# Performance work log

Hardware: AMD Instinct MI355X
Metric: run time of the kernel (lower is better)

Reference implementation:

```python
import jax, jax.numpy as jnp
import numpy as np

N_DRUG = 50000
N_DIS = 50000
N_EDGES = 500000
IN_UNITS = 4096   # rows of basis-decomposed weight (index vocab)
MSG_SMALL = 128   # msg_units(384) // 3 (ini=True)
OUT_UNITS = 256
BASIS_UNITS = 4
N_RATINGS = 2


def setup_inputs() -> dict:
    key = jax.random.key(0)
    ks = jax.random.split(key, 12)
    inp = {
        "drug_feat": jax.random.randint(ks[0], (N_DRUG, 3), 0, IN_UNITS, dtype=jnp.int32),
        "dis_feat": jax.random.randint(ks[1], (N_DIS, 3), 0, IN_UNITS, dtype=jnp.int32),
        # edge_src[r] = drug endpoint, edge_dst[r] = disease endpoint of rating-r edges
        "edge_src": jax.random.randint(ks[2], (N_RATINGS, N_EDGES), 0, N_DRUG, dtype=jnp.int32),
        "edge_dst": jax.random.randint(ks[3], (N_RATINGS, N_EDGES), 0, N_DIS, dtype=jnp.int32),
        # degree normalizers (graph.srcdata['cj'] / dstdata['ci'])
        "cj_drug": jax.random.uniform(ks[4], (N_DRUG, 1), dtype=jnp.float32),
        "ci_drug": jax.random.uniform(ks[5], (N_DRUG, 1), dtype=jnp.float32),
        "cj_dis": jax.random.uniform(ks[6], (N_DIS, 1), dtype=jnp.float32),
        "ci_dis": jax.random.uniform(ks[7], (N_DIS, 1), dtype=jnp.float32),
        # learned params (share_user_item_param=True -> ifc is ufc)
        "att": jax.random.normal(ks[8], (N_RATINGS, BASIS_UNITS), dtype=jnp.float32),
        "basis": jax.random.normal(ks[9], (BASIS_UNITS, IN_UNITS, MSG_SMALL), dtype=jnp.float32) * 0.02,
        "fc_w": jax.random.normal(ks[10], (OUT_UNITS, 3 * MSG_SMALL), dtype=jnp.float32) * 0.05,
        "fc_b": jnp.zeros((OUT_UNITS,), dtype=jnp.float32),
    }
    return inp


def _gather_feat(idx, Wr):
    # dot_or_identity: concat(W[idx0], W[idx1], W[idx2]) -> [N, 3*msg_small]
    g = Wr[idx]                      # [N, 3, msg_small]
    return g.reshape(idx.shape[0], -1)


def reference(drug_feat, dis_feat, edge_src, edge_dst, cj_drug, ci_drug,
              cj_dis, ci_dis, att, basis, fc_w, fc_b):
    # basis decomposition: W = att @ basis.view(B,-1) -> [R, in_units, msg_small]
    W = jnp.einsum('rb,bim->rim', att, basis)
    drug_out = jnp.zeros((cj_drug.shape[0], 3 * W.shape[2]), dtype=W.dtype)
    dis_out = jnp.zeros((cj_dis.shape[0], 3 * W.shape[2]), dtype=W.dtype)
    for r in range(att.shape[0]):
        Wr = W[r]
        src, dst = edge_src[r], edge_dst[r]
        # rating edges: drug -> disease (copy_src + sum, then * ci)
        h_drug = _gather_feat(drug_feat, Wr) * cj_drug
        dis_out = dis_out + jax.ops.segment_sum(h_drug[src], dst,
                                                num_segments=cj_dis.shape[0])
        # rev-rating edges: disease -> drug
        h_dis = _gather_feat(dis_feat, Wr) * cj_dis
        drug_out = drug_out + jax.ops.segment_sum(h_dis[dst], src,
                                                  num_segments=cj_drug.shape[0])
    dis_out = dis_out * ci_dis
    drug_out = drug_out * ci_drug
    # agg_act=None (identity), dropout_rate=0; shared output projection
    drug_out = drug_out @ fc_w.T + fc_b   # ifc
    dis_out = dis_out @ fc_w.T + fc_b     # ufc (shared params)
    return drug_out, dis_out
```

## Files before the change

### kernel.cpp

```cpp
#include <hip/hip_runtime.h>
#include <hip/hip_bf16.h>

#define N_NODE   50000
#define N_EDGES  500000
#define IN_UNITS 4096
#define MSG      128
#define OUT      256
#define N_RAT    2
#define CAP      64
#define NBKT     782
#define BCAP     2048
#define STAGE    8

typedef float f32x4 __attribute__((ext_vector_type(4)));

__device__ inline float bf2f(unsigned short u) {
    return __uint_as_float(((unsigned int)u) << 16);
}
__device__ inline unsigned short f2bf(float f) {
    unsigned int x = __float_as_uint(f);
    return (unsigned short)((x + 0x7fff + ((x >> 16) & 1)) >> 16);
}

__global__ void zero_kernel(int* p, int n) {
    int i = blockIdx.x * 256 + threadIdx.x;
    if (i < n) p[i] = 0;
}

__global__ void zw_kernel(const float* __restrict__ att,
                          const float* __restrict__ basis,
                          float* __restrict__ W,
                          int* __restrict__ bcnt) {
    int idx = blockIdx.x * 256 + threadIdx.x;
    if (blockIdx.x == 0) {
        for (int i = threadIdx.x; i < 2 * NBKT; i += 256) bcnt[i] = 0;
    }
    int r   = idx >> 19;
    int off = idx & 524287;
    float s = 0.f;
#pragma unroll
    for (int b = 0; b < 4; ++b)
        s += att[r * 4 + b] * basis[(size_t)b * 524288 + off];
    W[idx] = s;
}

template <typename OT>
__global__ __launch_bounds__(256) void p_kernel(const float* __restrict__ W,
                                                const float* __restrict__ fc_w,
                                                OT* __restrict__ P) {
    int t = blockIdx.z;
    int r = t / 3, k = t - r * 3;
    int i0 = blockIdx.y * 64;
    int o0 = blockIdx.x * 64;
    const float* A = W + (size_t)r * 4096 * 128;

    __shared__ float As[64][68];
    __shared__ float Bs[64][68];

    int tid = threadIdx.x;
    int tx = tid & 15, ty = tid >> 4;
    float acc[4][4] = {};

    for (int kk = 0; kk < 128; kk += 64) {
#pragma unroll
        for (int j = 0; j < 16; ++j) {
            int flat = tid + j * 256;
            int m = flat & 63, row = flat >> 6;
            As[m][row] = A[(size_t)(i0 + row) * 128 + kk + m];
            Bs[m][row] = fc_w[(size_t)(o0 + row) * 384 + k * 128 + kk + m];
        }
        __syncthreads();
#pragma unroll 8
        for (int m = 0; m < 64; ++m) {
            float4 a = *(const float4*)&As[m][ty * 4];
            float4 b = *(const float4*)&Bs[m][tx * 4];
            float av[4] = {a.x, a.y, a.z, a.w};
            float bv[4] = {b.x, b.y, b.z, b.w};
#pragma unroll
            for (int q = 0; q < 4; ++q)
#pragma unroll
                for (int p = 0; p < 4; ++p)
                    acc[q][p] += av[q] * bv[p];
        }
        __syncthreads();
    }
#pragma unroll
    for (int q = 0; q < 4; ++q) {
        size_t base = ((size_t)t * 4096 + i0 + ty * 4 + q) * 256 + o0 + tx * 4;
        if constexpr (sizeof(OT) == 4) {
            float4 v = make_float4(acc[q][0], acc[q][1], acc[q][2], acc[q][3]);
            *(float4*)&P[base] = v;
        } else {
            ushort4 v;
            v.x = f2bf(acc[q][0]); v.y = f2bf(acc[q][1]);
            v.z = f2bf(acc[q][2]); v.w = f2bf(acc[q][3]);
            *(ushort4*)&P[base] = v;
        }
    }
}

__global__ __launch_bounds__(256) void bin_kernel(
    const int* __restrict__ esrc, const int* __restrict__ edst,
    int* __restrict__ bcnt, int* __restrict__ bedges) {
    __shared__ int stage[2 * NBKT * STAGE];
    __shared__ int lcnt[2 * NBKT];
    int tid = threadIdx.x;
    for (int i = tid; i < 2 * NBKT; i += 256) lcnt[i] = 0;
    __syncthreads();

    const int EPB = (N_RAT * N_EDGES + gridDim.x - 1) / gridDim.x;
    int e0 = blockIdx.x * EPB;
    int e1 = e0 + EPB; if (e1 > N_RAT * N_EDGES) e1 = N_RAT * N_EDGES;

    for (int e = e0 + tid; e < e1; e += 256) {
        int r = (e >= N_EDGES) ? 1 : 0;
        int s = __builtin_nontemporal_load(esrc + e);
        int d = __builtin_nontemporal_load(edst + e);
        {
            int b = (s >> 6);
            int pay = d | (r << 16) | ((s & 63) << 17);
            int pos = atomicAdd(&lcnt[b], 1);
            if (pos < STAGE) stage[b * STAGE + pos] = pay;
            else { int gp = atomicAdd(&bcnt[b], 1);
                   if (gp < BCAP) bedges[(size_t)b * BCAP + gp] = pay; }
        }
        {
            int b = NBKT + (d >> 6);
            int pay = s | (r << 16) | ((d & 63) << 17);
            int pos = atomicAdd(&lcnt[b], 1);
            if (pos < STAGE) stage[b * STAGE + pos] = pay;
            else { int gp = atomicAdd(&bcnt[b], 1);
                   if (gp < BCAP) bedges[(size_t)b * BCAP + gp] = pay; }
        }
    }
    __syncthreads();
    for (int b = tid; b < 2 * NBKT; b += 256) {
        int n = lcnt[b]; if (n == 0) continue;
        if (n > STAGE) n = STAGE;
        int base = atomicAdd(&bcnt[b], n);
        for (int j = 0; j < n; ++j) {
            int pos = base + j;
            if (pos < BCAP) bedges[(size_t)b * BCAP + pos] = stage[b * STAGE + j];
        }
    }
}

__global__ __launch_bounds__(256) void hpre_kernel(
    const int* __restrict__ drug_feat, const int* __restrict__ dis_feat,
    const float* __restrict__ cj_drug, const float* __restrict__ cj_dis,
    const unsigned short* __restrict__ Pb, unsigned short* __restrict__ h) {
    int wave = blockIdx.x * 4 + (threadIdx.x >> 6);
    int lane = threadIdx.x & 63;
    if (wave >= 4 * N_NODE) return;
    int type = wave / (2 * N_NODE);
    int rem  = wave - type * 2 * N_NODE;
    int r    = rem / N_NODE;
    int node = rem - r * N_NODE;
    const int* feat = type ? dis_feat : drug_feat;
    float c = (type ? cj_dis : cj_drug)[node];
    int f0 = feat[node * 3 + 0];
    int f1 = feat[node * 3 + 1];
    int f2 = feat[node * 3 + 2];
    const ushort4* r0 = (const ushort4*)(Pb + (((size_t)(r * 3 + 0) * 4096 + f0) << 8));
    const ushort4* r1 = (const ushort4*)(Pb + (((size_t)(r * 3 + 1) * 4096 + f1) << 8));
    const ushort4* r2 = (const ushort4*)(Pb + (((size_t)(r * 3 + 2) * 4096 + f2) << 8));
    ushort4 a = r0[lane], b = r1[lane], d = r2[lane];
    ushort4 o;
    o.x = f2bf(c * (bf2f(a.x) + bf2f(b.x) + bf2f(d.x)));
    o.y = f2bf(c * (bf2f(a.y) + bf2f(b.y) + bf2f(d.y)));
    o.z = f2bf(c * (bf2f(a.z) + bf2f(b.z) + bf2f(d.z)));
    o.w = f2bf(c * (bf2f(a.w) + bf2f(b.w) + bf2f(d.w)));
    ((ushort4*)(h + ((size_t)wave << 8)))[lane] = o;
}

__global__ __launch_bounds__(256) void accum5_kernel(
    const int* __restrict__ bcnt, const int* __restrict__ bedges,
    const float* __restrict__ ci_drug, const float* __restrict__ ci_dis,
    const unsigned short* __restrict__ h, const float* __restrict__ fc_b,
    float* __restrict__ out) {
    __shared__ int slots[64][CAP];
    __shared__ int scnt[64];
    int tid = threadIdx.x;
    int b = blockIdx.x;
    int side = (b >= NBKT) ? 1 : 0;
    int bk = side ? b - NBKT : b;
    int node0 = bk * 64;

    if (tid < 64) scnt[tid] = 0;
    __syncthreads();

    int n = bcnt[b]; if (n > BCAP) n = BCAP;
    for (int i = tid; i < n; i += 256) {
        int pay = __builtin_nontemporal_load(bedges + (size_t)b * BCAP + i);
        int ln = (pay >> 17) & 63;
        int p = atomicAdd(&scnt[ln], 1);
        if (p < CAP) slots[ln][p] = pay;
    }
    __syncthreads();

    int wid = tid >> 6, lane = tid & 63;
    const float* ci = side ? ci_dis : ci_drug;
    int hoff = side ? 0 : 2 * N_NODE;
    float4 bv = ((const float4*)fc_b)[lane];

    for (int ln = wid; ln < 64; ln += 4) {
        int node = node0 + ln;
        if (node >= N_NODE) continue;
        int m = scnt[ln]; if (m > CAP) m = CAP;
        float4 acc = make_float4(0.f, 0.f, 0.f, 0.f);
        int j = 0;
        for (; j + 4 <= m; j += 4) {
            int p0 = slots[ln][j+0], p1 = slots[ln][j+1];
            int p2 = slots[ln][j+2], p3 = slots[ln][j+3];
            const ushort4* r0 = (const ushort4*)(h +
                ((size_t)(hoff + ((p0 >> 16) & 1) * N_NODE + (p0 & 0xFFFF)) << 8));
            const ushort4* r1 = (const ushort4*)(h +
                ((size_t)(hoff + ((p1 >> 16) & 1) * N_NODE + (p1 & 0xFFFF)) << 8));
            const ushort4* r2 = (const ushort4*)(h +
                ((size_t)(hoff + ((p2 >> 16) & 1) * N_NODE + (p2 & 0xFFFF)) << 8));
            const ushort4* r3 = (const ushort4*)(h +
                ((size_t)(hoff + ((p3 >> 16) & 1) * N_NODE + (p3 & 0xFFFF)) << 8));
            ushort4 v0 = r0[lane], v1 = r1[lane], v2 = r2[lane], v3 = r3[lane];
            acc.x += (bf2f(v0.x) + bf2f(v1.x)) + (bf2f(v2.x) + bf2f(v3.x));
            acc.y += (bf2f(v0.y) + bf2f(v1.y)) + (bf2f(v2.y) + bf2f(v3.y));
            acc.z += (bf2f(v0.z) + bf2f(v1.z)) + (bf2f(v2.z) + bf2f(v3.z));
            acc.w += (bf2f(v0.w) + bf2f(v1.w)) + (bf2f(v2.w) + bf2f(v3.w));
        }
        for (; j < m; ++j) {
            int pay = slots[ln][j];
            const ushort4* hr = (const ushort4*)(h +
                ((size_t)(hoff + ((pay >> 16) & 1) * N_NODE + (pay & 0xFFFF)) << 8));
            ushort4 v = hr[lane];
            acc.x += bf2f(v.x);
            acc.y += bf2f(v.y);
            acc.z += bf2f(v.z);
            acc.w += bf2f(v.w);
        }
        float civ = ci[node];
        float* orow = out + ((size_t)(side * N_NODE + node)) * 256;
        f32x4 res = {acc.x * civ + bv.x, acc.y * civ + bv.y,
                     acc.z * civ + bv.z, acc.w * civ + bv.w};
        __builtin_nontemporal_store(res, (f32x4*)orow + lane);
    }
}

__global__ void count_kernel(const int* __restrict__ esrc, const int* __restrict__ edst,
                             int* cnt_drug, int* cnt_dis) {
    int g = blockIdx.x * 256 + threadIdx.x;
    if (g >= N_RAT * N_EDGES) return;
    atomicAdd(&cnt_drug[esrc[g]], 1);
    atomicAdd(&cnt_dis[edst[g]], 1);
}

__global__ __launch_bounds__(1024) void scan_kernel(const int* cnt_drug, const int* cnt_dis,
                                                    int* offs_drug, int* offs_dis,
                                                    int* cur_drug, int* cur_dis) {
    const int n = N_NODE, chunk = 49;
    const int* cnt = blockIdx.x ? cnt_dis : cnt_drug;
    int* offs = blockIdx.x ? offs_dis : offs_drug;
    int* cur  = blockIdx.x ? cur_dis  : cur_drug;
    __shared__ int lds[1024];
    int t = threadIdx.x;
    int s = 0;
    int base = t * chunk;
    for (int j = 0; j < chunk; ++j) { int i = base + j; if (i < n) s += cnt[i]; }
    lds[t] = s;
    __syncthreads();
    for (int off = 1; off < 1024; off <<= 1) {
        int v = (t >= off) ? lds[t - off] : 0;
        __syncthreads();
        lds[t] += v;
        __syncthreads();
    }
    int run = lds[t] - s;
    for (int j = 0; j < chunk; ++j) {
        int i = base + j;
        if (i < n) { offs[i] = run; cur[i] = run; run += cnt[i]; }
    }
    if (t == 1023) offs[n] = lds[1023];
}

__global__ void scatter_kernel(const int* __restrict__ esrc, const int* __restrict__ edst,
                               int* cur_drug, int* cur_dis,
                               int* sorted_drug, int* sorted_dis) {
    int g = blockIdx.x * 256 + threadIdx.x;
    if (g >= N_RAT * N_EDGES) return;
    int r = (g >= N_EDGES) ? 1 : 0;
    int s = esrc[g], d = edst[g];
    int pd = atomicAdd(&cur_dis[d], 1);   sorted_dis[pd]  = s | (r << 16);
    int pu = atomicAdd(&cur_drug[s], 1);  sorted_drug[pu] = d | (r << 16);
}

__global__ __launch_bounds__(256) void accum_kernel(
    const int* __restrict__ sorted_drug, const int* __restrict__ sorted_dis,
    const int* __restrict__ offs_drug, const int* __restrict__ offs_dis,
    const int* __restrict__ drug_feat, const int* __restrict__ dis_feat,
    const float* __restrict__ cj_drug, const float* __restrict__ cj_dis,
    const float* __restrict__ ci_drug, const float* __restrict__ ci_dis,
    const float* __restrict__ P, const float* __restrict__ fc_b,
    float* __restrict__ out) {
    int wave = blockIdx.x * 4 + (threadIdx.x >> 6);
    int lane = threadIdx.x & 63;
    if (wave >= 2 * N_NODE) return;
    bool isDrug = wave < N_NODE;
    int node = isDrug ? wave : wave - N_NODE;

    const int *list, *feat;
    const float *cj, *ci;
    int s0, s1;
    float* orow;
    if (isDrug) {
        list = sorted_drug; s0 = offs_drug[node]; s1 = offs_drug[node + 1];
        feat = dis_feat; cj = cj_dis; ci = ci_drug;
        orow = out + (size_t)node * 256;
    } else {
        list = sorted_dis;  s0 = offs_dis[node];  s1 = offs_dis[node + 1];
        feat = drug_feat; cj = cj_drug; ci = ci_dis;
        orow = out + (size_t)(N_NODE + node) * 256;
    }

    float4 acc = make_float4(0.f, 0.f, 0.f, 0.f);
    for (int j = s0; j < s1; ++j) {
        int pay = list[j];
        int src = pay & 0xFFFF;
        int r   = pay >> 16;
        int f0 = feat[src * 3 + 0];
        int f1 = feat[src * 3 + 1];
        int f2 = feat[src * 3 + 2];
        float c = cj[src];
        const float4* r0 = (const float4*)(P + (((size_t)(r * 3 + 0) * 4096 + f0) << 8));
        const float4* r1 = (const float4*)(P + (((size_t)(r * 3 + 1) * 4096 + f1) << 8));
        const float4* r2 = (const float4*)(P + (((size_t)(r * 3 + 2) * 4096 + f2) << 8));
        float4 v0 = r0[lane], v1 = r1[lane], v2 = r2[lane];
        acc.x += c * (v0.x + v1.x + v2.x);
        acc.y += c * (v0.y + v1.y + v2.y);
        acc.z += c * (v0.z + v1.z + v2.z);
        acc.w += c * (v0.w + v1.w + v2.w);
    }
    float civ = ci[node];
    float4 b = ((const float4*)fc_b)[lane];
    float4 res = make_float4(acc.x * civ + b.x, acc.y * civ + b.y,
                             acc.z * civ + b.z, acc.w * civ + b.w);
    ((float4*)orow)[lane] = res;
}

extern "C" void kernel_launch(void* const* d_in, const int* in_sizes, int n_in,
                              void* d_out, int out_size, void* d_ws, size_t ws_size,
                              hipStream_t stream) {
    const int*   drug_feat = (const int*)  d_in[0];
    const int*   dis_feat  = (const int*)  d_in[1];
    const int*   edge_src  = (const int*)  d_in[2];
    const int*   edge_dst  = (const int*)  d_in[3];
    const float* cj_drug   = (const float*)d_in[4];
    const float* ci_drug   = (const float*)d_in[5];
    const float* cj_dis    = (const float*)d_in[6];
    const float* ci_dis    = (const float*)d_in[7];
    const float* att       = (const float*)d_in[8];
    const float* basis     = (const float*)d_in[9];
    const float* fc_w      = (const float*)d_in[10];
    const float* fc_b      = (const float*)d_in[11];
    float* out = (float*)d_out;
    char* ws = (char*)d_ws;

    const size_t BIN_NEED = 127803392;

    if (ws_size >= BIN_NEED) {
        unsigned short* Pb     = (unsigned short*)(ws + 0);
        unsigned short* h      = (unsigned short*)(ws + 12582912);
        float*          W      = (float*)         (ws + 12582912);
        int*            bcnt   = (int*)           (ws + 114982912);
        int*            bedges = (int*)           (ws + 114991104);

        zw_kernel<<<4096, 256, 0, stream>>>(att, basis, W, bcnt);
        bin_kernel<<<512, 256, 0, stream>>>(edge_src, edge_dst, bcnt, bedges);
        p_kernel<unsigned short><<<dim3(4, 64, 6), 256, 0, stream>>>(W, fc_w, Pb);
        hpre_kernel<<<(4 * N_NODE + 3) / 4, 256, 0, stream>>>(
            drug_feat, dis_feat, cj_drug, cj_dis, Pb, h);
        accum5_kernel<<<2 * NBKT, 256, 0, stream>>>(
            bcnt, bedges, ci_drug, ci_dis, h, fc_b, out);
    } else {
        float* W           = (float*)(ws + 0);
        float* P           = (float*)(ws + 4194304);
        int*   cnt_drug    = (int*)  (ws + 29360128);
        int*   cnt_dis     = (int*)  (ws + 29560128);
        int*   offs_drug   = (int*)  (ws + 29760128);
        int*   offs_dis    = (int*)  (ws + 29960144);
        int*   cur_drug    = (int*)  (ws + 30160160);
        int*   cur_dis     = (int*)  (ws + 30360160);
        int*   sorted_drug = (int*)  (ws + 30560160);
        int*   sorted_dis  = (int*)  (ws + 34560160);

        zero_kernel<<<(100000 + 255) / 256, 256, 0, stream>>>(cnt_drug, 100000);
        w_kernel_fallback:;
        zw_kernel<<<4096, 256, 0, stream>>>(att, basis, W, cnt_drug);
        zero_kernel<<<(100000 + 255) / 256, 256, 0, stream>>>(cnt_drug, 100000);
        p_kernel<float><<<dim3(4, 64, 6), 256, 0, stream>>>(W, fc_w, P);
        count_kernel<<<(N_RAT * N_EDGES + 255) / 256, 256, 0, stream>>>(
            edge_src, edge_dst, cnt_drug, cnt_dis);
        scan_kernel<<<2, 1024, 0, stream>>>(cnt_drug, cnt_dis, offs_drug, offs_dis,
                                            cur_drug, cur_dis);
        scatter_kernel<<<(N_RAT * N_EDGES + 255) / 256, 256, 0, stream>>>(
            edge_src, edge_dst, cur_drug, cur_dis, sorted_drug, sorted_dis);
        accum_kernel<<<(2 * N_NODE + 3) / 4, 256, 0, stream>>>(
            sorted_drug, sorted_dis, offs_drug, offs_dis,
            drug_feat, dis_feat, cj_drug, cj_dis, ci_drug, ci_dis,
            P, fc_b, out);
    }
}
```

Measured before the change: 298.8 us.

## Shrink buckets to 32 nodes and split hpre/accum per side for L2 reuse

```diff
diff --git a/kernel.cpp b/kernel.cpp
--- a/kernel.cpp
+++ b/kernel.cpp
@@ -8,9 +8,9 @@
 #define OUT      256
 #define N_RAT    2
 #define CAP      64
-#define NBKT     782
-#define BCAP     2048
-#define STAGE    8
+#define NB32     1563
+#define BC32     1024
+#define STG      4
 
 typedef float f32x4 __attribute__((ext_vector_type(4)));
 
@@ -32,8 +32,9 @@
                           float* __restrict__ W,
                           int* __restrict__ bcnt) {
     int idx = blockIdx.x * 256 + threadIdx.x;
-    if (blockIdx.x == 0) {
-        for (int i = threadIdx.x; i < 2 * NBKT; i += 256) bcnt[i] = 0;
+    if (blockIdx.x < 16) {
+        int z = blockIdx.x * 256 + threadIdx.x;
+        for (int i = z; i < 2 * NB32; i += 16 * 256) bcnt[i] = 0;
     }
     int r   = idx >> 19;
     int off = idx & 524287;
@@ -102,10 +103,10 @@
 __global__ __launch_bounds__(256) void bin_kernel(
     const int* __restrict__ esrc, const int* __restrict__ edst,
     int* __restrict__ bcnt, int* __restrict__ bedges) {
-    __shared__ int stage[2 * NBKT * STAGE];
-    __shared__ int lcnt[2 * NBKT];
+    __shared__ int stage[2 * NB32 * STG];
+    __shared__ int lcnt[2 * NB32];
     int tid = threadIdx.x;
-    for (int i = tid; i < 2 * NBKT; i += 256) lcnt[i] = 0;
+    for (int i = tid; i < 2 * NB32; i += 256) lcnt[i] = 0;
     __syncthreads();
 
     const int EPB = (N_RAT * N_EDGES + gridDim.x - 1) / gridDim.x;
@@ -117,47 +118,43 @@
         int s = __builtin_nontemporal_load(esrc + e);
         int d = __builtin_nontemporal_load(edst + e);
         {
-            int b = (s >> 6);
-            int pay = d | (r << 16) | ((s & 63) << 17);
+            int b = (s >> 5);
+            int pay = d | (r << 16) | ((s & 31) << 17);
             int pos = atomicAdd(&lcnt[b], 1);
-            if (pos < STAGE) stage[b * STAGE + pos] = pay;
+            if (pos < STG) stage[b * STG + pos] = pay;
             else { int gp = atomicAdd(&bcnt[b], 1);
-                   if (gp < BCAP) bedges[(size_t)b * BCAP + gp] = pay; }
+                   if (gp < BC32) bedges[(size_t)b * BC32 + gp] = pay; }
         }
         {
-            int b = NBKT + (d >> 6);
-            int pay = s | (r << 16) | ((d & 63) << 17);
+            int b = NB32 + (d >> 5);
+            int pay = s | (r << 16) | ((d & 31) << 17);
             int pos = atomicAdd(&lcnt[b], 1);
-            if (pos < STAGE) stage[b * STAGE + pos] = pay;
+            if (pos < STG) stage[b * STG + pos] = pay;
             else { int gp = atomicAdd(&bcnt[b], 1);
-                   if (gp < BCAP) bedges[(size_t)b * BCAP + gp] = pay; }
+                   if (gp < BC32) bedges[(size_t)b * BC32 + gp] = pay; }
         }
     }
     __syncthreads();
-    for (int b = tid; b < 2 * NBKT; b += 256) {
+    for (int b = tid; b < 2 * NB32; b += 256) {
         int n = lcnt[b]; if (n == 0) continue;
-        if (n > STAGE) n = STAGE;
+        if (n > STG) n = STG;
         int base = atomicAdd(&bcnt[b], n);
         for (int j = 0; j < n; ++j) {
             int pos = base + j;
-            if (pos < BCAP) bedges[(size_t)b * BCAP + pos] = stage[b * STAGE + j];
-        }
-    }
-}
-
-__global__ __launch_bounds__(256) void hpre_kernel(
-    const int* __restrict__ drug_feat, const int* __restrict__ dis_feat,
-    const float* __restrict__ cj_drug, const float* __restrict__ cj_dis,
-    const unsigned short* __restrict__ Pb, unsigned short* __restrict__ h) {
+            if (pos < BC32) bedges[(size_t)b * BC32 + pos] = stage[b * STG + j];
+        }
+    }
+}
+
+__global__ __launch_bounds__(256) void hpre_half_kernel(
+    const int* __restrict__ feat, const float* __restrict__ cj,
+    const unsigned short* __restrict__ Pb, unsigned short* __restrict__ h_half) {
     int wave = blockIdx.x * 4 + (threadIdx.x >> 6);
     int lane = threadIdx.x & 63;
-    if (wave >= 4 * N_NODE) return;
-    int type = wave / (2 * N_NODE);
-    int rem  = wave - type * 2 * N_NODE;
-    int r    = rem / N_NODE;
-    int node = rem - r * N_NODE;
-    const int* feat = type ? dis_feat : drug_feat;
-    float c = (type ? cj_dis : cj_drug)[node];
+    if (wave >= 2 * N_NODE) return;
+    int r    = wave / N_NODE;
+    int node = wave - r * N_NODE;
+    float c = cj[node];
     int f0 = feat[node * 3 + 0];
     int f1 = feat[node * 3 + 1];
     int f2 = feat[node * 3 + 2];
@@ -170,40 +167,35 @@
     o.y = f2bf(c * (bf2f(a.y) + bf2f(b.y) + bf2f(d.y)));
     o.z = f2bf(c * (bf2f(a.z) + bf2f(b.z) + bf2f(d.z)));
     o.w = f2bf(c * (bf2f(a.w) + bf2f(b.w) + bf2f(d.w)));
-    ((ushort4*)(h + ((size_t)wave << 8)))[lane] = o;
-}
-
-__global__ __launch_bounds__(256) void accum5_kernel(
+    ((ushort4*)(h_half + ((size_t)wave << 8)))[lane] = o;
+}
+
+__global__ __launch_bounds__(256) void accum_side_kernel(
     const int* __restrict__ bcnt, const int* __restrict__ bedges,
-    const float* __restrict__ ci_drug, const float* __restrict__ ci_dis,
-    const unsigned short* __restrict__ h, const float* __restrict__ fc_b,
-    float* __restrict__ out) {
-    __shared__ int slots[64][CAP];
-    __shared__ int scnt[64];
+    const float* __restrict__ ci, const unsigned short* __restrict__ h_half,
+    const float* __restrict__ fc_b, float* __restrict__ out_half) {
+    __shared__ int slots[32][CAP];
+    __shared__ int scnt[32];
     int tid = threadIdx.x;
-    int b = blockIdx.x;
-    int side = (b >= NBKT) ? 1 : 0;
-    int bk = side ? b - NBKT : b;
-    int node0 = bk * 64;
-
-    if (tid < 64) scnt[tid] = 0;
+    int bk = blockIdx.x;
+    int node0 = bk * 32;
+
+    if (tid < 32) scnt[tid] = 0;
     __syncthreads();
 
-    int n = bcnt[b]; if (n > BCAP) n = BCAP;
+    int n = bcnt[bk]; if (n > BC32) n = BC32;
     for (int i = tid; i < n; i += 256) {
-        int pay = __builtin_nontemporal_load(bedges + (size_t)b * BCAP + i);
-        int ln = (pay >> 17) & 63;
+        int pay = __builtin_nontemporal_load(bedges + (size_t)bk * BC32 + i);
+        int ln = (pay >> 17) & 31;
         int p = atomicAdd(&scnt[ln], 1);
         if (p < CAP) slots[ln][p] = pay;
     }
     __syncthreads();
 
     int wid = tid >> 6, lane = tid & 63;
-    const float* ci = side ? ci_dis : ci_drug;
-    int hoff = side ? 0 : 2 * N_NODE;
     float4 bv = ((const float4*)fc_b)[lane];
 
-    for (int ln = wid; ln < 64; ln += 4) {
+    for (int ln = wid; ln < 32; ln += 4) {
         int node = node0 + ln;
         if (node >= N_NODE) continue;
         int m = scnt[ln]; if (m > CAP) m = CAP;
@@ -212,14 +204,14 @@
         for (; j + 4 <= m; j += 4) {
             int p0 = slots[ln][j+0], p1 = slots[ln][j+1];
             int p2 = slots[ln][j+2], p3 = slots[ln][j+3];
-            const ushort4* r0 = (const ushort4*)(h +
-                ((size_t)(hoff + ((p0 >> 16) & 1) * N_NODE + (p0 & 0xFFFF)) << 8));
-            const ushort4* r1 = (const ushort4*)(h +
-                ((size_t)(hoff + ((p1 >> 16) & 1) * N_NODE + (p1 & 0xFFFF)) << 8));
-            const ushort4* r2 = (const ushort4*)(h +
-                ((size_t)(hoff + ((p2 >> 16) & 1) * N_NODE + (p2 & 0xFFFF)) << 8));
-            const ushort4* r3 = (const ushort4*)(h +
-                ((size_t)(hoff + ((p3 >> 16) & 1) * N_NODE + (p3 & 0xFFFF)) << 8));
+            const ushort4* r0 = (const ushort4*)(h_half +
+                ((size_t)(((p0 >> 16) & 1) * N_NODE + (p0 & 0xFFFF)) << 8));
+            const ushort4* r1 = (const ushort4*)(h_half +
+                ((size_t)(((p1 >> 16) & 1) * N_NODE + (p1 & 0xFFFF)) << 8));
+            const ushort4* r2 = (const ushort4*)(h_half +
+                ((size_t)(((p2 >> 16) & 1) * N_NODE + (p2 & 0xFFFF)) << 8));
+            const ushort4* r3 = (const ushort4*)(h_half +
+                ((size_t)(((p3 >> 16) & 1) * N_NODE + (p3 & 0xFFFF)) << 8));
             ushort4 v0 = r0[lane], v1 = r1[lane], v2 = r2[lane], v3 = r3[lane];
             acc.x += (bf2f(v0.x) + bf2f(v1.x)) + (bf2f(v2.x) + bf2f(v3.x));
             acc.y += (bf2f(v0.y) + bf2f(v1.y)) + (bf2f(v2.y) + bf2f(v3.y));
@@ -228,8 +220,8 @@
         }
         for (; j < m; ++j) {
             int pay = slots[ln][j];
-            const ushort4* hr = (const ushort4*)(h +
-                ((size_t)(hoff + ((pay >> 16) & 1) * N_NODE + (pay & 0xFFFF)) << 8));
+            const ushort4* hr = (const ushort4*)(h_half +
+                ((size_t)(((pay >> 16) & 1) * N_NODE + (pay & 0xFFFF)) << 8));
             ushort4 v = hr[lane];
             acc.x += bf2f(v.x);
             acc.y += bf2f(v.y);
@@ -237,11 +229,24 @@
             acc.w += bf2f(v.w);
         }
         float civ = ci[node];
-        float* orow = out + ((size_t)(side * N_NODE + node)) * 256;
+        float* orow = out_half + (size_t)node * 256;
         f32x4 res = {acc.x * civ + bv.x, acc.y * civ + bv.y,
                      acc.z * civ + bv.z, acc.w * civ + bv.w};
         __builtin_nontemporal_store(res, (f32x4*)orow + lane);
     }
+}
+
+__global__ void w_kernel(const float* __restrict__ att,
+                         const float* __restrict__ basis,
+                         float* __restrict__ W) {
+    int idx = blockIdx.x * 256 + threadIdx.x;
+    int r   = idx >> 19;
+    int off = idx & 524287;
+    float s = 0.f;
+#pragma unroll
+    for (int b = 0; b < 4; ++b)
+        s += att[r * 4 + b] * basis[(size_t)b * 524288 + off];
+    W[idx] = s;
 }
 
 __global__ void count_kernel(const int* __restrict__ esrc, const int* __restrict__ edst,
@@ -369,15 +374,23 @@
         unsigned short* h      = (unsigned short*)(ws + 12582912);
         float*          W      = (float*)         (ws + 12582912);
         int*            bcnt   = (int*)           (ws + 114982912);
-        int*            bedges = (int*)           (ws + 114991104);
+        int*            bedges = (int*)           (ws + 114999296);
+
+        unsigned short* h0 = h;
+        unsigned short* h1 = h + (size_t)2 * N_NODE * 256;
 
         zw_kernel<<<4096, 256, 0, stream>>>(att, basis, W, bcnt);
         bin_kernel<<<512, 256, 0, stream>>>(edge_src, edge_dst, bcnt, bedges);
         p_kernel<unsigned short><<<dim3(4, 64, 6), 256, 0, stream>>>(W, fc_w, Pb);
-        hpre_kernel<<<(4 * N_NODE + 3) / 4, 256, 0, stream>>>(
-            drug_feat, dis_feat, cj_drug, cj_dis, Pb, h);
-        accum5_kernel<<<2 * NBKT, 256, 0, stream>>>(
-            bcnt, bedges, ci_drug, ci_dis, h, fc_b, out);
+        hpre_half_kernel<<<(2 * N_NODE + 3) / 4, 256, 0, stream>>>(
+            dis_feat, cj_dis, Pb, h1);
+        accum_side_kernel<<<NB32, 256, 0, stream>>>(
+            bcnt, bedges, ci_drug, h1, fc_b, out);
+        hpre_half_kernel<<<(2 * N_NODE + 3) / 4, 256, 0, stream>>>(
+            drug_feat, cj_drug, Pb, h0);
+        accum_side_kernel<<<NB32, 256, 0, stream>>>(
+            bcnt + NB32, bedges + (size_t)NB32 * BC32, ci_dis, h0, fc_b,
+            out + (size_t)N_NODE * 256);
     } else {
         float* W           = (float*)(ws + 0);
         float* P           = (float*)(ws + 4194304);
@@ -391,9 +404,7 @@
         int*   sorted_dis  = (int*)  (ws + 34560160);
 
         zero_kernel<<<(100000 + 255) / 256, 256, 0, stream>>>(cnt_drug, 100000);
-        w_kernel_fallback:;
-        zw_kernel<<<4096, 256, 0, stream>>>(att, basis, W, cnt_drug);
-        zero_kernel<<<(100000 + 255) / 256, 256, 0, stream>>>(cnt_drug, 100000);
+        w_kernel<<<1048576 / 256, 256, 0, stream>>>(att, basis, W);
         p_kernel<float><<<dim3(4, 64, 6), 256, 0, stream>>>(W, fc_w, P);
         count_kernel<<<(N_RAT * N_EDGES + 255) / 256, 256, 0, stream>>>(
             edge_src, edge_dst, cnt_drug, cnt_dis);
```

Result: slower. 310.1 us (+3.8%).
